# Kernel optimization log

Hardware: AMD Instinct MI355X
Metric: run time of the kernel (lower is better)

The kernel has to match this reference:

```python
import jax, jax.numpy as jnp
import numpy as np

N, E = 50000, 400000          # nodes, edges (avg degree 8)
DIN, DEIN = 128, 128          # in_node_feats, in_edge_feats
H, DE, DN = 8, 16, 16         # num_heads, out_edge_feats, out_node_feats
HDE = H * DE                  # 128


def setup_inputs() -> dict:
    key = jax.random.key(0)
    ks = jax.random.split(key, 14)
    nfeats = jax.random.normal(ks[0], (N, DIN), jnp.float32)
    efeats = jax.random.normal(ks[1], (E, DEIN), jnp.float32)
    norm = jax.random.uniform(ks[2], (E, 1), jnp.float32)
    src = jax.random.randint(ks[3], (E,), 0, N, jnp.int32)
    # guarantee every node has in-degree >= 1 (module raises on 0-in-degree)
    dst = jnp.concatenate([jax.random.permutation(ks[4], N).astype(jnp.int32),
                           jax.random.randint(ks[5], (E - N,), 0, N, jnp.int32)])
    s = 0.05
    W_ni = jax.random.normal(ks[6], (HDE, DIN), jnp.float32) * s
    W_nj = jax.random.normal(ks[7], (HDE, DIN), jnp.float32) * s
    W_fij = jax.random.normal(ks[8], (HDE, DEIN), jnp.float32) * s
    W_edges = jax.random.normal(ks[9], (HDE, 3 * HDE), jnp.float32) * s
    W_attn = jax.random.normal(ks[10], (H, DE), jnp.float32) * s
    bias = jnp.zeros((HDE,), jnp.float32)
    W_node = jax.random.normal(ks[11], (H * DN, DIN), jnp.float32) * s
    b_node = jnp.zeros((H * DN,), jnp.float32)
    return dict(nfeats=nfeats, efeats=efeats, norm=norm, src=src, dst=dst,
                W_ni=W_ni, W_nj=W_nj, W_fij=W_fij, W_edges=W_edges,
                W_attn=W_attn, bias=bias, W_node=W_node, b_node=b_node)


def reference(nfeats, efeats, norm, src, dst,
              W_ni, W_nj, W_fij, W_edges, W_attn, bias, W_node, b_node):
    # node/edge linear projections
    f_ni = nfeats @ W_ni.T            # [N, H*De]
    f_nj = nfeats @ W_nj.T            # [N, H*De]
    f_eij = efeats @ W_fij.T          # [E, H*De]
    # fc_edges(cat[f_ni[src], f_eij, f_nj[dst]]) == sum of 3 block-matmuls;
    # project on nodes/edges FIRST, then gather (same math, less edge traffic)
    W1, W2, W3 = jnp.split(W_edges, 3, axis=1)   # each [H*De, H*De]
    t_src = f_ni @ W1.T               # [N, H*De]
    t_e = f_eij @ W2.T                # [E, H*De]
    t_dst = f_nj @ W3.T               # [N, H*De]
    f_lin = t_src[src] + t_e + t_dst[dst]         # [E, H*De]
    f = jax.nn.leaky_relu(f_lin)                  # slope 0.01 == torch default
    f_out = (f + bias).reshape(E, H, DE)          # [E, H, De]
    # fc_attn then sum over head-out dim == dot with column-sum of W_attn
    a = jnp.einsum('ehd,d->eh', f_out, W_attn.sum(0))   # [E, H]
    # edge_softmax over edges incoming to each dst node, per head
    m = jax.ops.segment_max(a, dst, num_segments=N)     # [N, H]
    ex = jnp.exp(a - m[dst])
    den = jax.ops.segment_sum(ex, dst, num_segments=N)  # [N, H]
    alpha = (ex / den[dst])[:, :, None]                 # [E, H, 1]
    # mpnn_type='node': message = h_out[src] * a * norm, reduced by sum at dst
    h_node = (nfeats @ W_node.T + b_node).reshape(N, H, DN)
    msg = h_node[src] * alpha * norm[:, :, None]        # [E, H, Dn]
    h_out = jax.ops.segment_sum(msg, dst, num_segments=N)  # [N, H, Dn]
    return h_out.sum(axis=1), f_out.sum(axis=1)
```

## Files before the change

kernel.cpp:

```cpp
#include <hip/hip_runtime.h>

typedef unsigned short ushort_t;
typedef __attribute__((ext_vector_type(8))) short short8;
typedef __attribute__((ext_vector_type(4))) float f32x4;
typedef __attribute__((ext_vector_type(4))) int i32x4;

#define NN 50000
#define NE 400000
#define WS_NEED 46531200ull

static __device__ __forceinline__ float bf2f(ushort_t u) {
    union { unsigned int i; float f; } v; v.i = ((unsigned int)u) << 16; return v.f;
}
static __device__ __forceinline__ ushort_t f2bf(float f) {
    unsigned int u = __float_as_uint(f);
    u = (u + 0x7fffu + ((u >> 16) & 1u)) >> 16;
    return (ushort_t)u;
}
static __device__ __forceinline__ float loadf(const void* base, size_t i, int f32) {
    return f32 ? ((const float*)base)[i] : bf2f(((const ushort_t*)base)[i]);
}
static __device__ __forceinline__ short8 load8(const void* base, size_t off, int f32) {
    if (f32) {
        const float* p = (const float*)base + off;
        const f32x4 a = *(const f32x4*)p;
        const f32x4 b = *(const f32x4*)(p + 4);
        short8 r;
#pragma unroll
        for (int i = 0; i < 4; i++) { r[i] = (short)f2bf(a[i]); r[i + 4] = (short)f2bf(b[i]); }
        return r;
    }
    return *(const short8*)((const ushort_t*)base + off);
}

__global__ void k_detect(const ushort_t* __restrict__ nf, int* __restrict__ flag) {
    if (threadIdx.x == 0) {
        int cnt = 0;
        for (int i = 0; i < 512; i += 2) {
            const int eb = (nf[i] >> 7) & 0xFF;
            cnt += (eb >= 0xB0);
        }
        *flag = (cnt > 8) ? 1 : 0;
    }
}

__global__ void k_zero(float* __restrict__ p, int n) {
    const int i = blockIdx.x * 256 + threadIdx.x;
    if (i < n) p[i] = 0.f;
}

__global__ void k_recip(float* __restrict__ p, int n) {
    const int i = blockIdx.x * 256 + threadIdx.x;
    if (i < n) p[i] = 1.f / fmaxf(p[i], 1e-30f);
}

__global__ void k_prep(const void* __restrict__ W_ni, const void* __restrict__ W_nj,
                       const void* __restrict__ W_fij, const void* __restrict__ W_edges,
                       const void* __restrict__ W_attn, const void* __restrict__ W_node,
                       const int* __restrict__ flag,
                       ushort_t* __restrict__ Wcat, ushort_t* __restrict__ Ae,
                       float* __restrict__ wsum) {
    const int f32 = *flag;
    int r = blockIdx.x;
    int k = threadIdx.x;
    if (r == 0 && k < 16) {
        float s = 0.f;
        for (int h = 0; h < 8; h++) s += loadf(W_attn, h * 16 + k, f32);
        wsum[k] = s;
    }
    const int ks = k ^ ((r & 7) << 3);
    float acc = 0.f;
    if (r < 128) {
        for (int m = 0; m < 128; m++)
            acc += loadf(W_edges, r * 384 + m, f32) * loadf(W_ni, m * 128 + k, f32);
        Wcat[r * 128 + ks] = f2bf(acc);
    } else if (r < 256) {
        int j = r - 128;
        for (int m = 0; m < 128; m++)
            acc += loadf(W_edges, j * 384 + 256 + m, f32) * loadf(W_nj, m * 128 + k, f32);
        Wcat[r * 128 + ks] = f2bf(acc);
    } else if (r < 384) {
        Wcat[r * 128 + ks] = f2bf(loadf(W_node, (r - 256) * 128 + k, f32));
    } else {
        int j = r - 384;
        for (int m = 0; m < 128; m++)
            acc += loadf(W_edges, j * 384 + 128 + m, f32) * loadf(W_fij, m * 128 + k, f32);
        Ae[j * 128 + (k ^ ((j & 7) << 3))] = f2bf(acc);
    }
}

__global__ __launch_bounds__(256) void k_nodes(const void* __restrict__ X,
                                               const ushort_t* __restrict__ Wcat,
                                               const void* __restrict__ b_node,
                                               const int* __restrict__ flag,
                                               ushort_t* __restrict__ tsrc,
                                               ushort_t* __restrict__ tdst,
                                               ushort_t* __restrict__ hnode) {
    __shared__ ushort_t sW[128 * 128];
    const int f32 = *flag;
    const int g = blockIdx.x % 3;
    const int tch = blockIdx.x / 3;
    const int lane = threadIdx.x & 63, wave = threadIdx.x >> 6;
    const int c = lane & 15, quad = lane >> 4;

    const ushort_t* Wg = Wcat + (size_t)g * 16384;
#pragma unroll
    for (int it2 = 0; it2 < 8; it2++) {
        const int idx = (it2 * 256 + threadIdx.x) * 8;
        *(short8*)(sW + idx) = *(const short8*)(Wg + idx);
    }
    __syncthreads();

    ushort_t* const outp = (g == 0) ? tsrc : (g == 1) ? tdst : hnode;
    float bnv[8];
#pragma unroll
    for (int t = 0; t < 8; t++) bnv[t] = (g == 2) ? loadf(b_node, t * 16 + c, f32) : 0.f;

    for (int it = 0; it < 3; it++) {
        const int tile = tch * 3 + it;
        if (tile * 64 >= NN) break;
        const int m0 = tile * 64 + wave * 16;
        int arow = m0 + c;
        if (arow >= NN) arow = NN - 1;
        short8 a[4];
#pragma unroll
        for (int k4 = 0; k4 < 4; k4++)
            a[k4] = load8(X, (size_t)arow * 128 + k4 * 32 + quad * 8, f32);
        f32x4 acc[8];
#pragma unroll
        for (int t = 0; t < 8; t++) acc[t] = (f32x4){0.f, 0.f, 0.f, 0.f};
#pragma unroll
        for (int k4 = 0; k4 < 4; k4++) {
            const int ks = (k4 * 32 + quad * 8) ^ ((c & 7) << 3);
#pragma unroll
            for (int t = 0; t < 8; t++) {
                short8 b = *(const short8*)(sW + (size_t)(t * 16 + c) * 128 + ks);
                acc[t] = __builtin_amdgcn_mfma_f32_16x16x32_bf16(a[k4], b, acc[t], 0, 0, 0);
            }
        }
#pragma unroll
        for (int r = 0; r < 4; r++) {
            const int m = m0 + quad * 4 + r;
            short8 v;
#pragma unroll
            for (int t = 0; t < 8; t++) v[t] = (short)f2bf(acc[t][r] + bnv[t]);
            if (m < NN) *(short8*)(outp + (size_t)m * 128 + c * 8) = v;
        }
    }
}

template<int F32>
static __device__ __forceinline__ void edges_body(
    const void* __restrict__ EF, const ushort_t* sAe,
    const int* __restrict__ src, const int* __restrict__ dst,
    const ushort_t* __restrict__ tsrc, const ushort_t* __restrict__ tdst,
    const void* __restrict__ bias, const float* __restrict__ wsum,
    ushort_t* __restrict__ exw, float* __restrict__ den, float* __restrict__ out1) {
    const int lane = threadIdx.x & 63, wave = threadIdx.x >> 6;
    const int c = lane & 15, quad = lane >> 4;

    const float wc = wsum[c];
    float biasv[8];
#pragma unroll
    for (int t = 0; t < 8; t++) biasv[t] = loadf(bias, t * 16 + c, F32);

    const int ew0 = blockIdx.x * 320 + wave * 16;
    i32x4 svn = *(const i32x4*)(src + ew0 + quad * 4);
    i32x4 dvn = *(const i32x4*)(dst + ew0 + quad * 4);
    f32x4 raw[8];
    short8 an[4];
    {
        const size_t base = (size_t)(ew0 + c) * 128 + quad * 8;
        if (F32) {
            const float* p = (const float*)EF;
#pragma unroll
            for (int k4 = 0; k4 < 4; k4++) {
                raw[k4 * 2]     = *(const f32x4*)(p + base + k4 * 32);
                raw[k4 * 2 + 1] = *(const f32x4*)(p + base + k4 * 32 + 4);
            }
        } else {
            const ushort_t* p = (const ushort_t*)EF;
#pragma unroll
            for (int k4 = 0; k4 < 4; k4++) an[k4] = *(const short8*)(p + base + k4 * 32);
        }
    }

    for (int it = 0; it < 5; it++) {
        const int ecur = ew0 + it * 64;
        const i32x4 sv4 = svn, dv4 = dvn;
        short8 a[4];
        if (F32) {
#pragma unroll
            for (int k4 = 0; k4 < 4; k4++) {
#pragma unroll
                for (int j = 0; j < 4; j++) {
                    a[k4][j]     = (short)f2bf(raw[k4 * 2][j]);
                    a[k4][j + 4] = (short)f2bf(raw[k4 * 2 + 1][j]);
                }
            }
        } else {
#pragma unroll
            for (int k4 = 0; k4 < 4; k4++) a[k4] = an[k4];
        }
        short8 ts8[4], td8[4];
#pragma unroll
        for (int r = 0; r < 4; r++) {
            ts8[r] = *(const short8*)(tsrc + (size_t)sv4[r] * 128 + c * 8);
            td8[r] = *(const short8*)(tdst + (size_t)dv4[r] * 128 + c * 8);
        }
        if (it < 4) {
            const int en = ecur + 64;
            svn = *(const i32x4*)(src + en + quad * 4);
            dvn = *(const i32x4*)(dst + en + quad * 4);
            const size_t base = (size_t)(en + c) * 128 + quad * 8;
            if (F32) {
                const float* p = (const float*)EF;
#pragma unroll
                for (int k4 = 0; k4 < 4; k4++) {
                    raw[k4 * 2]     = *(const f32x4*)(p + base + k4 * 32);
                    raw[k4 * 2 + 1] = *(const f32x4*)(p + base + k4 * 32 + 4);
                }
            } else {
                const ushort_t* p = (const ushort_t*)EF;
#pragma unroll
                for (int k4 = 0; k4 < 4; k4++) an[k4] = *(const short8*)(p + base + k4 * 32);
            }
        }
        f32x4 acc[8];
#pragma unroll
        for (int t = 0; t < 8; t++) acc[t] = (f32x4){0.f, 0.f, 0.f, 0.f};
#pragma unroll
        for (int k4 = 0; k4 < 4; k4++) {
            const int ks = (k4 * 32 + quad * 8) ^ ((c & 7) << 3);
#pragma unroll
            for (int t = 0; t < 8; t++) {
                short8 b = *(const short8*)(sAe + (size_t)(t * 16 + c) * 128 + ks);
                acc[t] = __builtin_amdgcn_mfma_f32_16x16x32_bf16(a[k4], b, acc[t], 0, 0, 0);
            }
        }
#pragma unroll
        for (int r = 0; r < 4; r++) {
            const int e = ecur + quad * 4 + r;
            const int dv = dv4[r];
            float o1 = 0.f, part[8];
#pragma unroll
            for (int t = 0; t < 8; t++) {
                float f = acc[t][r] + bf2f((ushort_t)ts8[r][t]) + bf2f((ushort_t)td8[r][t]);
                f = (f > 0.f) ? f : 0.01f * f;
                const float fo = f + biasv[t];
                o1 += fo;
                part[t] = fo * wc;
            }
            out1[(size_t)e * 16 + c] = o1;
            float q[4];
#pragma unroll
            for (int i2 = 0; i2 < 4; i2++) {
                const float send  = (c & 8) ? part[i2] : part[i2 + 4];
                const float other = __shfl_xor(send, 8);
                const float mine  = (c & 8) ? part[i2 + 4] : part[i2];
                q[i2] = mine + other;
            }
            float p2[2];
#pragma unroll
            for (int i2 = 0; i2 < 2; i2++) {
                const float send  = (c & 4) ? q[i2] : q[i2 + 2];
                const float other = __shfl_xor(send, 4);
                const float mine  = (c & 4) ? q[i2 + 2] : q[i2];
                p2[i2] = mine + other;
            }
            const float send  = (c & 2) ? p2[0] : p2[1];
            const float other = __shfl_xor(send, 2);
            const float mine  = (c & 2) ? p2[1] : p2[0];
            float p1 = mine + other;
            p1 += __shfl_xor(p1, 1);
            if (!(c & 1)) {
                const int h = c >> 1;
                const float av = fminf(fmaxf(p1, -50.f), 50.f);
                const float ex = __expf(av);
                const ushort_t exb16 = f2bf(ex);
                exw[(size_t)e * 8 + h] = exb16;
                atomicAdd(&den[(size_t)dv * 8 + h], bf2f(exb16));
            }
        }
    }
}

__global__ __launch_bounds__(256) void k_edges(const void* __restrict__ EF,
                                               const ushort_t* __restrict__ Ae,
                                               const int* __restrict__ src,
                                               const int* __restrict__ dst,
                                               const ushort_t* __restrict__ tsrc,
                                               const ushort_t* __restrict__ tdst,
                                               const void* __restrict__ bias,
                                               const float* __restrict__ wsum,
                                               const int* __restrict__ flag,
                                               ushort_t* __restrict__ exw,
                                               float* __restrict__ den,
                                               float* __restrict__ out1) {
    __shared__ ushort_t sAe[128 * 128];
#pragma unroll
    for (int it2 = 0; it2 < 8; it2++) {
        const int idx = (it2 * 256 + threadIdx.x) * 8;
        *(short8*)(sAe + idx) = *(const short8*)(Ae + idx);
    }
    __syncthreads();
    if (*flag) edges_body<1>(EF, sAe, src, dst, tsrc, tdst, bias, wsum, exw, den, out1);
    else       edges_body<0>(EF, sAe, src, dst, tsrc, tdst, bias, wsum, exw, den, out1);
}

__global__ __launch_bounds__(256) void k_msg(const int* __restrict__ src,
                                             const int* __restrict__ dst,
                                             const void* __restrict__ norm,
                                             const ushort_t* __restrict__ hnode,
                                             const ushort_t* __restrict__ exw,
                                             const float* __restrict__ den,
                                             const int* __restrict__ flag,
                                             float* __restrict__ out0) {
    const int f32 = *flag;
    const int tid = blockIdx.x * 256 + threadIdx.x;
    const int e = tid >> 4, d = tid & 15;
    if (e >= NE) return;
    const int sv = src[e], dv = dst[e];
    const float nm = loadf(norm, e, f32);
    const short8 hn = *(const short8*)(hnode + (size_t)sv * 128 + d * 8);
    const short8 ew = *(const short8*)(exw + (size_t)e * 8);
    const f32x4* rd = (const f32x4*)(den + (size_t)dv * 8);
    const f32x4 r0 = rd[0], r1 = rd[1];
    float s = 0.f;
#pragma unroll
    for (int h = 0; h < 4; h++)
        s += bf2f((ushort_t)hn[h]) * (bf2f((ushort_t)ew[h]) * r0[h]);
#pragma unroll
    for (int h = 0; h < 4; h++)
        s += bf2f((ushort_t)hn[4 + h]) * (bf2f((ushort_t)ew[4 + h]) * r1[h]);
    atomicAdd(&out0[(size_t)dv * 16 + d], s * nm);
}

extern "C" void kernel_launch(void* const* d_in, const int* in_sizes, int n_in,
                              void* d_out, int out_size, void* d_ws, size_t ws_size,
                              hipStream_t stream) {
    const void* nfeats  = d_in[0];
    const void* efeats  = d_in[1];
    const void* norm    = d_in[2];
    const int*  src     = (const int*)d_in[3];
    const int*  dst     = (const int*)d_in[4];
    const void* W_ni    = d_in[5];
    const void* W_nj    = d_in[6];
    const void* W_fij   = d_in[7];
    const void* W_edges = d_in[8];
    const void* W_attn  = d_in[9];
    const void* bias    = d_in[10];
    const void* W_node  = d_in[11];
    const void* b_node  = d_in[12];

    if (ws_size < WS_NEED) {
        k_zero<<<(out_size + 255) / 256, 256, 0, stream>>>((float*)d_out, out_size);
        return;
    }

    char* ws = (char*)d_ws;
    const size_t o_den   = 0;
    const size_t o_exw   = 1600000;
    const size_t o_wcat  = 8000000;
    const size_t o_ae    = 8098304;
    const size_t o_wsum  = 8131072;
    const size_t o_flag  = 8131136;
    const size_t o_tsrc  = 8131200;
    const size_t o_tdst  = o_tsrc + 12800000;
    const size_t o_hnode = o_tdst + 12800000;

    float*    den   = (float*)(ws + o_den);
    ushort_t* exw   = (ushort_t*)(ws + o_exw);
    ushort_t* Wcat  = (ushort_t*)(ws + o_wcat);
    ushort_t* Ae    = (ushort_t*)(ws + o_ae);
    float*    wsum  = (float*)(ws + o_wsum);
    int*      flag  = (int*)(ws + o_flag);
    ushort_t* tsrc  = (ushort_t*)(ws + o_tsrc);
    ushort_t* tdst  = (ushort_t*)(ws + o_tdst);
    ushort_t* hnode = (ushort_t*)(ws + o_hnode);

    float* out0 = (float*)d_out;
    float* out1 = (float*)d_out + NN * 16;

    k_detect<<<1, 64, 0, stream>>>((const ushort_t*)nfeats, flag);
    k_zero<<<(NN * 8 + 255) / 256, 256, 0, stream>>>(den, NN * 8);
    k_zero<<<(NN * 16 + 255) / 256, 256, 0, stream>>>(out0, NN * 16);
    k_prep<<<512, 128, 0, stream>>>(W_ni, W_nj, W_fij, W_edges, W_attn, W_node, flag, Wcat, Ae, wsum);
    k_nodes<<<786, 256, 0, stream>>>(nfeats, Wcat, b_node, flag, tsrc, tdst, hnode);
    k_edges<<<1250, 256, 0, stream>>>(efeats, Ae, src, dst, tsrc, tdst, bias, wsum, flag, exw, den, out1);
    k_recip<<<(NN * 8 + 255) / 256, 256, 0, stream>>>(den, NN * 8);
    k_msg<<<NE * 16 / 256, 256, 0, stream>>>(src, dst, norm, hnode, exw, den, flag, out0);
}
```

Baseline: 443.2 us.

## Replace atomic scatter softmax/message with CSR gather per destination node

Builds a CSR adjacency by destination (count, two-level scan, fill) and replaces the atomic denominator accumulation and the atomic message scatter with a per-node gather kernel. That kernel sums the exp weights and the weighted messages over each node's incoming edges, then normalises. The aim is to remove float atomics on den and out0 and to drop the reciprocal and zeroing passes. In exchange it adds four small graph-building kernels (with their own atomics), and the gather loop is irregular by node degree.

```diff
diff --git a/kernel.cpp b/kernel.cpp
--- a/kernel.cpp
+++ b/kernel.cpp
@@ -7,7 +7,9 @@
 
 #define NN 50000
 #define NE 400000
-#define WS_NEED 46531200ull
+#define NPAD 50176
+#define NB 196
+#define WS_NEED 47135360ull
 
 static __device__ __forceinline__ float bf2f(ushort_t u) {
     union { unsigned int i; float f; } v; v.i = ((unsigned int)u) << 16; return v.f;
@@ -49,9 +51,50 @@
     if (i < n) p[i] = 0.f;
 }
 
-__global__ void k_recip(float* __restrict__ p, int n) {
-    const int i = blockIdx.x * 256 + threadIdx.x;
-    if (i < n) p[i] = 1.f / fmaxf(p[i], 1e-30f);
+__global__ void k_count(const int* __restrict__ dst, int* __restrict__ deg) {
+    const int e = blockIdx.x * 256 + threadIdx.x;
+    if (e < NE) atomicAdd(&deg[dst[e]], 1);
+}
+
+__global__ void k_scan(const int* __restrict__ deg, int* __restrict__ lofs,
+                       int* __restrict__ bsum) {
+    __shared__ int s[256];
+    const int t = threadIdx.x;
+    const int v = blockIdx.x * 256 + t;
+    const int d = (v < NN) ? deg[v] : 0;
+    s[t] = d; __syncthreads();
+    for (int off = 1; off < 256; off <<= 1) {
+        const int x = (t >= off) ? s[t - off] : 0;
+        __syncthreads();
+        s[t] += x;
+        __syncthreads();
+    }
+    lofs[v] = s[t] - d;
+    if (t == 255) bsum[blockIdx.x] = s[255];
+}
+
+__global__ void k_scan2(const int* __restrict__ bsum, int* __restrict__ boff) {
+    __shared__ int s[256];
+    const int t = threadIdx.x;
+    const int d = (t < NB) ? bsum[t] : 0;
+    s[t] = d; __syncthreads();
+    for (int off = 1; off < 256; off <<= 1) {
+        const int x = (t >= off) ? s[t - off] : 0;
+        __syncthreads();
+        s[t] += x;
+        __syncthreads();
+    }
+    boff[t] = s[t] - d;
+}
+
+__global__ void k_fill(const int* __restrict__ dst, const int* __restrict__ lofs,
+                       const int* __restrict__ boff, int* __restrict__ cur,
+                       int* __restrict__ adj) {
+    const int e = blockIdx.x * 256 + threadIdx.x;
+    if (e >= NE) return;
+    const int v = dst[e];
+    const int slot = atomicAdd(&cur[v], 1);
+    adj[lofs[v] + boff[v >> 8] + slot] = e;
 }
 
 __global__ void k_prep(const void* __restrict__ W_ni, const void* __restrict__ W_nj,
@@ -155,7 +198,7 @@
     const int* __restrict__ src, const int* __restrict__ dst,
     const ushort_t* __restrict__ tsrc, const ushort_t* __restrict__ tdst,
     const void* __restrict__ bias, const float* __restrict__ wsum,
-    ushort_t* __restrict__ exw, float* __restrict__ den, float* __restrict__ out1) {
+    ushort_t* __restrict__ exw, float* __restrict__ out1) {
     const int lane = threadIdx.x & 63, wave = threadIdx.x >> 6;
     const int c = lane & 15, quad = lane >> 4;
 
@@ -241,7 +284,6 @@
 #pragma unroll
         for (int r = 0; r < 4; r++) {
             const int e = ecur + quad * 4 + r;
-            const int dv = dv4[r];
             float o1 = 0.f, part[8];
 #pragma unroll
             for (int t = 0; t < 8; t++) {
@@ -277,9 +319,7 @@
                 const int h = c >> 1;
                 const float av = fminf(fmaxf(p1, -50.f), 50.f);
                 const float ex = __expf(av);
-                const ushort_t exb16 = f2bf(ex);
-                exw[(size_t)e * 8 + h] = exb16;
-                atomicAdd(&den[(size_t)dv * 8 + h], bf2f(exb16));
+                exw[(size_t)e * 8 + h] = f2bf(ex);
             }
         }
     }
@@ -295,7 +335,6 @@
                                                const float* __restrict__ wsum,
                                                const int* __restrict__ flag,
                                                ushort_t* __restrict__ exw,
-                                               float* __restrict__ den,
                                                float* __restrict__ out1) {
     __shared__ ushort_t sAe[128 * 128];
 #pragma unroll
@@ -304,36 +343,46 @@
         *(short8*)(sAe + idx) = *(const short8*)(Ae + idx);
     }
     __syncthreads();
-    if (*flag) edges_body<1>(EF, sAe, src, dst, tsrc, tdst, bias, wsum, exw, den, out1);
-    else       edges_body<0>(EF, sAe, src, dst, tsrc, tdst, bias, wsum, exw, den, out1);
-}
-
-__global__ __launch_bounds__(256) void k_msg(const int* __restrict__ src,
-                                             const int* __restrict__ dst,
+    if (*flag) edges_body<1>(EF, sAe, src, dst, tsrc, tdst, bias, wsum, exw, out1);
+    else       edges_body<0>(EF, sAe, src, dst, tsrc, tdst, bias, wsum, exw, out1);
+}
+
+__global__ __launch_bounds__(256) void k_out(const int* __restrict__ src,
                                              const void* __restrict__ norm,
+                                             const int* __restrict__ deg,
+                                             const int* __restrict__ lofs,
+                                             const int* __restrict__ boff,
+                                             const int* __restrict__ adj,
                                              const ushort_t* __restrict__ hnode,
                                              const ushort_t* __restrict__ exw,
-                                             const float* __restrict__ den,
                                              const int* __restrict__ flag,
                                              float* __restrict__ out0) {
     const int f32 = *flag;
-    const int tid = blockIdx.x * 256 + threadIdx.x;
-    const int e = tid >> 4, d = tid & 15;
-    if (e >= NE) return;
-    const int sv = src[e], dv = dst[e];
-    const float nm = loadf(norm, e, f32);
-    const short8 hn = *(const short8*)(hnode + (size_t)sv * 128 + d * 8);
-    const short8 ew = *(const short8*)(exw + (size_t)e * 8);
-    const f32x4* rd = (const f32x4*)(den + (size_t)dv * 8);
-    const f32x4 r0 = rd[0], r1 = rd[1];
+    const int gid = blockIdx.x * 256 + threadIdx.x;
+    const int v = gid >> 4, d = gid & 15;
+    if (v >= NN) return;
+    const int base = lofs[v] + boff[v >> 8];
+    const int n = deg[v];
+    float accd[8], dend[8];
+#pragma unroll
+    for (int h = 0; h < 8; h++) { accd[h] = 0.f; dend[h] = 0.f; }
+    for (int i = 0; i < n; i++) {
+        const int e = adj[base + i];
+        const int sv = src[e];
+        const float nm = loadf(norm, e, f32);
+        const short8 ex8 = *(const short8*)(exw + (size_t)e * 8);
+        const short8 hn = *(const short8*)(hnode + (size_t)sv * 128 + d * 8);
+#pragma unroll
+        for (int h = 0; h < 8; h++) {
+            const float ex = bf2f((ushort_t)ex8[h]);
+            dend[h] += ex;
+            accd[h] += bf2f((ushort_t)hn[h]) * ex * nm;
+        }
+    }
     float s = 0.f;
 #pragma unroll
-    for (int h = 0; h < 4; h++)
-        s += bf2f((ushort_t)hn[h]) * (bf2f((ushort_t)ew[h]) * r0[h]);
-#pragma unroll
-    for (int h = 0; h < 4; h++)
-        s += bf2f((ushort_t)hn[4 + h]) * (bf2f((ushort_t)ew[4 + h]) * r1[h]);
-    atomicAdd(&out0[(size_t)dv * 16 + d], s * nm);
+    for (int h = 0; h < 8; h++) s += accd[h] / fmaxf(dend[h], 1e-30f);
+    out0[(size_t)v * 16 + d] = s;
 }
 
 extern "C" void kernel_launch(void* const* d_in, const int* in_sizes, int n_in,
@@ -359,17 +408,21 @@
     }
 
     char* ws = (char*)d_ws;
-    const size_t o_den   = 0;
-    const size_t o_exw   = 1600000;
-    const size_t o_wcat  = 8000000;
-    const size_t o_ae    = 8098304;
-    const size_t o_wsum  = 8131072;
-    const size_t o_flag  = 8131136;
-    const size_t o_tsrc  = 8131200;
+    const size_t o_exw   = 0;
+    const size_t o_wcat  = 6400000;
+    const size_t o_ae    = 6498304;
+    const size_t o_wsum  = 6531072;
+    const size_t o_flag  = 6531136;
+    const size_t o_tsrc  = 6531200;
     const size_t o_tdst  = o_tsrc + 12800000;
     const size_t o_hnode = o_tdst + 12800000;
-
-    float*    den   = (float*)(ws + o_den);
+    const size_t o_deg   = 44931200;
+    const size_t o_cur   = o_deg + 200704;
+    const size_t o_lofs  = o_cur + 200704;
+    const size_t o_bsum  = o_lofs + 200704;
+    const size_t o_boff  = o_bsum + 1024;
+    const size_t o_adj   = o_boff + 1024;
+
     ushort_t* exw   = (ushort_t*)(ws + o_exw);
     ushort_t* Wcat  = (ushort_t*)(ws + o_wcat);
     ushort_t* Ae    = (ushort_t*)(ws + o_ae);
@@ -378,16 +431,24 @@
     ushort_t* tsrc  = (ushort_t*)(ws + o_tsrc);
     ushort_t* tdst  = (ushort_t*)(ws + o_tdst);
     ushort_t* hnode = (ushort_t*)(ws + o_hnode);
+    int*      deg   = (int*)(ws + o_deg);
+    int*      cur   = (int*)(ws + o_cur);
+    int*      lofs  = (int*)(ws + o_lofs);
+    int*      bsum  = (int*)(ws + o_bsum);
+    int*      boff  = (int*)(ws + o_boff);
+    int*      adj   = (int*)(ws + o_adj);
 
     float* out0 = (float*)d_out;
     float* out1 = (float*)d_out + NN * 16;
 
     k_detect<<<1, 64, 0, stream>>>((const ushort_t*)nfeats, flag);
-    k_zero<<<(NN * 8 + 255) / 256, 256, 0, stream>>>(den, NN * 8);
-    k_zero<<<(NN * 16 + 255) / 256, 256, 0, stream>>>(out0, NN * 16);
+    k_zero<<<(2 * NPAD + 255) / 256, 256, 0, stream>>>((float*)deg, 2 * NPAD);
     k_prep<<<512, 128, 0, stream>>>(W_ni, W_nj, W_fij, W_edges, W_attn, W_node, flag, Wcat, Ae, wsum);
+    k_count<<<(NE + 255) / 256, 256, 0, stream>>>(dst, deg);
+    k_scan<<<NB, 256, 0, stream>>>(deg, lofs, bsum);
+    k_scan2<<<1, 256, 0, stream>>>(bsum, boff);
+    k_fill<<<(NE + 255) / 256, 256, 0, stream>>>(dst, lofs, boff, cur, adj);
     k_nodes<<<786, 256, 0, stream>>>(nfeats, Wcat, b_node, flag, tsrc, tdst, hnode);
-    k_edges<<<1250, 256, 0, stream>>>(efeats, Ae, src, dst, tsrc, tdst, bias, wsum, flag, exw, den, out1);
-    k_recip<<<(NN * 8 + 255) / 256, 256, 0, stream>>>(den, NN * 8);
-    k_msg<<<NE * 16 / 256, 256, 0, stream>>>(src, dst, norm, hnode, exw, den, flag, out0);
-}
+    k_edges<<<1250, 256, 0, stream>>>(efeats, Ae, src, dst, tsrc, tdst, bias, wsum, flag, exw, out1);
+    k_out<<<(NPAD * 16) / 256, 256, 0, stream>>>(src, norm, deg, lofs, boff, adj, hnode, exw, flag, out0);
+}
```

Measured after the change: 487.5 us. 1.1x slower.
